# Kernel tuning notes

Measured on AMD Instinct MI355X. Metric: run time of the kernel, lower is better.

The kernel has to match this reference:

```python
import jax, jax.numpy as jnp
import numpy as np

B, T, D_MODEL = 2, 1024, 512
EXPAND = 2
D_INNER = D_MODEL * EXPAND
STATE = 16
K_CONV = 4


def setup_inputs() -> dict:
    key = jax.random.key(0)
    ks = jax.random.split(key, 10)
    sc = lambda k, shape: jax.random.normal(k, shape, jnp.float32) * 0.02
    return {
        "x": jax.random.normal(ks[0], (B, T, D_MODEL), jnp.float32),
        "ln_g": jnp.ones((D_MODEL,), jnp.float32),
        "ln_b": jnp.zeros((D_MODEL,), jnp.float32),
        "W_in": sc(ks[1], (2 * D_INNER, D_MODEL)),
        "conv_w": sc(ks[2], (D_INNER, 1, K_CONV)),
        "conv_b": jnp.zeros((D_INNER,), jnp.float32),
        "W_B": sc(ks[3], (STATE, D_INNER)),
        "W_C": sc(ks[4], (STATE, D_INNER)),
        "W_dt": sc(ks[5], (D_INNER, D_INNER)),
        "b_dt": jax.random.uniform(ks[6], (D_INNER,), jnp.float32, -4.0, -1.0),
        # log_A init: A_diag = -(n+1) from HiPPO, log(-A_diag) = log(n+1), broadcast over d_inner
        "log_A": jnp.broadcast_to(jnp.log(jnp.arange(1, STATE + 1, dtype=jnp.float32)), (D_INNER, STATE)),
        "W_out": sc(ks[7], (D_MODEL, D_INNER)),
    }


def _silu(v):
    return v * jax.nn.sigmoid(v)


def reference(x, ln_g, ln_b, W_in, conv_w, conv_b, W_B, W_C, W_dt, b_dt, log_A, W_out):
    residual = x
    # LayerNorm (biased variance, eps=1e-5)
    mu = x.mean(-1, keepdims=True)
    var = x.var(-1, keepdims=True)
    xn = (x - mu) * jax.lax.rsqrt(var + 1e-5) * ln_g + ln_b
    # input projection and gate split
    xz = xn @ W_in.T                      # (B,T,2*D_INNER)
    x_main, z = jnp.split(xz, 2, axis=-1)
    # depthwise causal conv1d (padding=3 then slice to T == left-pad 3)
    xc = jnp.transpose(x_main, (0, 2, 1))  # (B,D_INNER,T)
    xc = jax.lax.conv_general_dilated(
        xc, conv_w, window_strides=(1,), padding=[(K_CONV - 1, 0)],
        dimension_numbers=("NCH", "OIH", "NCH"), feature_group_count=D_INNER,
    ) + conv_b[None, :, None]
    x_main = _silu(jnp.transpose(xc, (0, 2, 1)))  # (B,T,D_INNER)
    # selective scan in fp32
    xf = x_main.astype(jnp.float32)
    Bt = xf @ W_B.T                        # (B,T,N)
    Ct = xf @ W_C.T                        # (B,T,N)
    dt = jax.nn.softplus(xf @ W_dt.T + b_dt)  # (B,T,D_INNER)
    A = -jnp.exp(log_A)                    # (D_INNER,N)
    dA = jnp.exp(A[None, None] * dt[..., None])              # (B,T,D_INNER,N)
    dBx = dt[..., None] * Bt[:, :, None, :] * xf[..., None]  # (B,T,D_INNER,N)

    def comb(c1, c2):
        a1, b1 = c1
        a2, b2 = c2
        return a1 * a2, a2 * b1 + b2

    _, h = jax.lax.associative_scan(comb, (dA, dBx), axis=1)  # h_t = dA_t*h_{t-1}+dBx_t
    y = (h * Ct[:, :, None, :]).sum(-1).astype(x.dtype)       # (B,T,D_INNER)
    out = (y * _silu(z)) @ W_out.T
    return residual + out
```

## Files before the change

kernel.cpp:

```cpp
#include <hip/hip_runtime.h>

#define T_SEQ 1024
#define DM 512
#define DI 1024
#define NS 16
#define NC 64
#define CL 16

typedef __attribute__((ext_vector_type(8))) short short8;
typedef __attribute__((ext_vector_type(4))) float f32x4;
typedef unsigned short u16;
typedef unsigned int u32;

__device__ inline float b2f(u16 u) {
    unsigned v = ((unsigned)u) << 16;
    return __builtin_bit_cast(float, v);
}
__device__ inline u16 f2b(float f) {
    unsigned u = __builtin_bit_cast(unsigned, f);
    u += 0x7fff + ((u >> 16) & 1);
    return (u16)(u >> 16);
}

__device__ inline void g2l16(const u16* g, short* l) {
    __builtin_amdgcn_global_load_lds((const __attribute__((address_space(1))) u32*)g,
                                     (__attribute__((address_space(3))) u32*)l, 16, 0, 0);
}

__global__ __launch_bounds__(256) void prep_k(const float* __restrict__ Win, const float* __restrict__ Wdt,
                       const float* __restrict__ Wout, const float* __restrict__ Wb,
                       const float* __restrict__ Wc,
                       u16* __restrict__ oWin, u16* __restrict__ oWdt, u16* __restrict__ oWout,
                       u16* __restrict__ oWb, u16* __restrict__ oWc,
                       const float* __restrict__ x, const float* __restrict__ g,
                       const float* __restrict__ be, u16* __restrict__ xn) {
    if (blockIdx.x < 2592) {
        int i = blockIdx.x * 256 + threadIdx.x;
        const float* s; u16* d; int off;
        if (i < 262144)      { s = Win;  d = oWin;  off = i; }
        else if (i < 524288) { s = Wdt;  d = oWdt;  off = i - 262144; }
        else if (i < 655360) { s = Wout; d = oWout; off = i - 524288; }
        else if (i < 659456) { s = Wb;   d = oWb;   off = i - 655360; }
        else                 { s = Wc;   d = oWc;   off = i - 659456; }
        float4 v = ((const float4*)s)[off];
        d[off * 4 + 0] = f2b(v.x);
        d[off * 4 + 1] = f2b(v.y);
        d[off * 4 + 2] = f2b(v.z);
        d[off * 4 + 3] = f2b(v.w);
        return;
    }
    int row = blockIdx.x - 2592, tid = threadIdx.x;
    float2 v = ((const float2*)(x + row * DM))[tid];
    float s = v.x + v.y, q = v.x * v.x + v.y * v.y;
    #pragma unroll
    for (int m = 1; m < 64; m <<= 1) { s += __shfl_xor(s, m); q += __shfl_xor(q, m); }
    __shared__ float ss[4], qq[4];
    if ((tid & 63) == 0) { ss[tid >> 6] = s; qq[tid >> 6] = q; }
    __syncthreads();
    s = ss[0] + ss[1] + ss[2] + ss[3];
    q = qq[0] + qq[1] + qq[2] + qq[3];
    float mu = s / DM;
    float var = q / DM - mu * mu;
    float rs = rsqrtf(var + 1e-5f);
    int c = tid * 2;
    xn[row * DM + c]     = f2b((v.x - mu) * rs * g[c] + be[c]);
    xn[row * DM + c + 1] = f2b((v.y - mu) * rs * g[c + 1] + be[c + 1]);
}

template<int BM, int BN, int NT, int EPI>
__global__ __launch_bounds__(256) void gemm_bt(const u16* __restrict__ A, int lda,
                                               const u16* __restrict__ Bw, int ldb,
                                               void* __restrict__ outp, int ldo,
                                               const float* __restrict__ extra) {
    __shared__ short a_sh[2][BM * 64];
    __shared__ short b_sh[2][BN * 64];
    constexpr int MI = BM / 32, NJ = BN / 32;
    int tid = threadIdx.x, w = tid >> 6, lane = tid & 63;
    int m0 = blockIdx.x * BM, n0 = blockIdx.y * BN;
    int wr = (w >> 1) * (BM / 2), wc = (w & 1) * (BN / 2);
    int lr = lane & 15, kg = lane >> 4;
    f32x4 acc[MI][NJ] = {};
    const u16* Abase = A + (size_t)m0 * lda;
    const u16* Bbase = Bw + (size_t)n0 * ldb;
    int lrow = lane >> 3;
    int lchunk = lane & 7;
    int schunk = lchunk ^ lrow;

    auto stage = [&](int cur, int kt) {
        int k0 = kt * 64;
        #pragma unroll
        for (int r = 0; r < BM / 32; ++r) {
            int row = r * 32 + w * 8 + lrow;
            g2l16(Abase + (size_t)row * lda + k0 + schunk * 8,
                  &a_sh[cur][(r * 32 + w * 8) * 64 + lane * 8]);
        }
        #pragma unroll
        for (int r = 0; r < BN / 32; ++r) {
            int row = r * 32 + w * 8 + lrow;
            g2l16(Bbase + (size_t)row * ldb + k0 + schunk * 8,
                  &b_sh[cur][(r * 32 + w * 8) * 64 + lane * 8]);
        }
    };

    stage(0, 0);
    __syncthreads();
    int cur = 0;
    for (int t = 0; t < NT; ++t) {
        if (t + 1 < NT) stage(cur ^ 1, t + 1);
        #pragma unroll
        for (int kk = 0; kk < 2; ++kk) {
            short8 af[MI], bfr[NJ];
            #pragma unroll
            for (int i = 0; i < MI; ++i) {
                int row = wr + i * 16 + lr;
                af[i] = *(const short8*)&a_sh[cur][row * 64 + (((kk << 2) | kg) ^ (row & 7)) * 8];
            }
            #pragma unroll
            for (int j = 0; j < NJ; ++j) {
                int row = wc + j * 16 + lr;
                bfr[j] = *(const short8*)&b_sh[cur][row * 64 + (((kk << 2) | kg) ^ (row & 7)) * 8];
            }
            #pragma unroll
            for (int i = 0; i < MI; ++i)
                #pragma unroll
                for (int j = 0; j < NJ; ++j)
                    acc[i][j] = __builtin_amdgcn_mfma_f32_16x16x32_bf16(af[i], bfr[j], acc[i][j], 0, 0, 0);
        }
        __syncthreads();
        cur ^= 1;
    }

    int rb = (lane >> 4) * 4, cc = lane & 15;
    #pragma unroll
    for (int i = 0; i < MI; ++i) {
        #pragma unroll
        for (int j = 0; j < NJ; ++j) {
            #pragma unroll
            for (int r = 0; r < 4; ++r) {
                int row = m0 + wr + i * 16 + rb + r;
                int col = n0 + wc + j * 16 + cc;
                float v = acc[i][j][r];
                if (EPI == 0) {
                    ((u16*)outp)[(size_t)row * ldo + col] = f2b(v);
                } else if (EPI == 1) {
                    float xx = v + extra[col];
                    float sp = (xx > 20.f) ? xx : log1pf(__expf(xx));
                    ((u16*)outp)[(size_t)row * ldo + col] = f2b(sp);
                } else {
                    ((float*)outp)[(size_t)row * ldo + col] = v + extra[(size_t)row * ldo + col];
                }
            }
        }
    }
}

__global__ void conv_k(const u16* __restrict__ xz, const float* __restrict__ w,
                       const float* __restrict__ cb, u16* __restrict__ xf) {
    int idx = blockIdx.x * 256 + threadIdx.x;
    int d = idx & (DI - 1);
    int bt = idx >> 10;
    int t = bt & (T_SEQ - 1);
    float s = cb[d];
    #pragma unroll
    for (int i = 0; i < 4; ++i) {
        int tt = t - 3 + i;
        if (tt >= 0) s += w[d * 4 + i] * b2f(xz[(size_t)(bt - 3 + i) * 2048 + d]);
    }
    float sig = 1.f / (1.f + __expf(-s));
    xf[idx] = f2b(s * sig);
}

__global__ __launch_bounds__(256) void bc_k(const u16* __restrict__ xf, const u16* __restrict__ Wb,
                                            const u16* __restrict__ Wc,
                                            float* __restrict__ Bt, float* __restrict__ Ct) {
    int m = blockIdx.x * 8 + (threadIdx.x >> 5);
    int j = threadIdx.x & 31;
    const u16* wrow = (j < 16) ? (Wb + j * DI) : (Wc + (j - 16) * DI);
    const short8* xr = (const short8*)(xf + (size_t)m * DI);
    const short8* wr = (const short8*)wrow;
    float s = 0.f;
    #pragma unroll 4
    for (int k = 0; k < DI / 8; ++k) {
        short8 a = xr[k], b = wr[k];
        #pragma unroll
        for (int e = 0; e < 8; ++e) s += b2f((u16)a[e]) * b2f((u16)b[e]);
    }
    float* o = (j < 16) ? Bt : Ct;
    o[(size_t)m * NS + (j & 15)] = s;
}

__global__ __launch_bounds__(256) void scanA(const u16* __restrict__ dt, const u16* __restrict__ xf,
                                             const float* __restrict__ Bt, const float* __restrict__ logA,
                                             float* __restrict__ Aprod, float* __restrict__ S) {
    int tid = threadIdx.x;
    int dblk = blockIdx.x & 3;
    int c = (blockIdx.x >> 2) & (NC - 1);
    int b = blockIdx.x >> 8;
    int d = dblk * 256 + tid;
    float Adn[NS], ap[NS], h[NS];
    #pragma unroll
    for (int j = 0; j < 4; ++j)
        *(float4*)&Adn[j * 4] = ((const float4*)(logA + (size_t)d * NS))[j];
    #pragma unroll
    for (int n = 0; n < NS; ++n) { Adn[n] = -__expf(Adn[n]); ap[n] = 1.f; h[n] = 0.f; }
    const u16* dtp = dt + ((size_t)b * T_SEQ + c * CL) * DI + d;
    const u16* xfp = xf + ((size_t)b * T_SEQ + c * CL) * DI + d;
    const float* Bp = Bt + ((size_t)b * T_SEQ + c * CL) * NS;
    #pragma unroll
    for (int i = 0; i < CL; ++i) {
        float dtv = b2f(dtp[(size_t)i * DI]);
        float xv  = b2f(xfp[(size_t)i * DI]);
        float ux = dtv * xv;
        float Bv[NS];
        #pragma unroll
        for (int j = 0; j < 4; ++j) *(float4*)&Bv[j * 4] = ((const float4*)(Bp + (size_t)i * NS))[j];
        #pragma unroll
        for (int n = 0; n < NS; ++n) {
            float dA = __expf(Adn[n] * dtv);
            h[n] = fmaf(dA, h[n], ux * Bv[n]);
            ap[n] *= dA;
        }
    }
    size_t o = ((((size_t)c * 2 + b) * DI) + d) * NS;
    #pragma unroll
    for (int j = 0; j < 4; ++j) {
        ((float4*)(Aprod + o))[j] = *(float4*)&ap[j * 4];
        ((float4*)(S + o))[j]     = *(float4*)&h[j * 4];
    }
}

__global__ __launch_bounds__(256) void scanB(const float* __restrict__ Aprod, const float* __restrict__ S,
                                             float* __restrict__ Hin) {
    int chain = blockIdx.x * 256 + threadIdx.x;
    float h = 0.f;
    #pragma unroll 8
    for (int c = 0; c < NC; ++c) {
        size_t o = (size_t)c * 32768 + chain;
        Hin[o] = h;
        h = fmaf(Aprod[o], h, S[o]);
    }
}

__global__ __launch_bounds__(256) void scanC(const u16* __restrict__ dt, const u16* __restrict__ xf,
                                             const float* __restrict__ Bt, const float* __restrict__ Ct,
                                             const float* __restrict__ logA, const float* __restrict__ Hin,
                                             const u16* __restrict__ xz, u16* __restrict__ ym) {
    int tid = threadIdx.x;
    int dblk = blockIdx.x & 3;
    int c = (blockIdx.x >> 2) & (NC - 1);
    int b = blockIdx.x >> 8;
    int d = dblk * 256 + tid;
    float Adn[NS], h[NS];
    #pragma unroll
    for (int j = 0; j < 4; ++j)
        *(float4*)&Adn[j * 4] = ((const float4*)(logA + (size_t)d * NS))[j];
    #pragma unroll
    for (int n = 0; n < NS; ++n) Adn[n] = -__expf(Adn[n]);
    size_t o = ((((size_t)c * 2 + b) * DI) + d) * NS;
    #pragma unroll
    for (int j = 0; j < 4; ++j) *(float4*)&h[j * 4] = ((const float4*)(Hin + o))[j];
    const u16* dtp = dt + ((size_t)b * T_SEQ + c * CL) * DI + d;
    const u16* xfp = xf + ((size_t)b * T_SEQ + c * CL) * DI + d;
    const float* Bp = Bt + ((size_t)b * T_SEQ + c * CL) * NS;
    const float* Cp = Ct + ((size_t)b * T_SEQ + c * CL) * NS;
    const u16* zp = xz + ((size_t)b * T_SEQ + c * CL) * 2048 + 1024 + d;
    u16* yp = ym + ((size_t)b * T_SEQ + c * CL) * DI + d;
    #pragma unroll
    for (int i = 0; i < CL; ++i) {
        float dtv = b2f(dtp[(size_t)i * DI]);
        float xv  = b2f(xfp[(size_t)i * DI]);
        float ux = dtv * xv;
        float Bv[NS], Cv[NS];
        #pragma unroll
        for (int j = 0; j < 4; ++j) {
            *(float4*)&Bv[j * 4] = ((const float4*)(Bp + (size_t)i * NS))[j];
            *(float4*)&Cv[j * 4] = ((const float4*)(Cp + (size_t)i * NS))[j];
        }
        float r = 0.f;
        #pragma unroll
        for (int n = 0; n < NS; ++n) {
            float dA = __expf(Adn[n] * dtv);
            h[n] = fmaf(dA, h[n], ux * Bv[n]);
            r = fmaf(h[n], Cv[n], r);
        }
        float zv = b2f(zp[(size_t)i * 2048]);
        float sz = zv / (1.f + __expf(-zv));
        yp[(size_t)i * DI] = f2b(r * sz);
    }
}

extern "C" void kernel_launch(void* const* d_in, const int* in_sizes, int n_in,
                              void* d_out, int out_size, void* d_ws, size_t ws_size,
                              hipStream_t stream) {
    const float* x     = (const float*)d_in[0];
    const float* ln_g  = (const float*)d_in[1];
    const float* ln_b  = (const float*)d_in[2];
    const float* W_in  = (const float*)d_in[3];
    const float* conv_w= (const float*)d_in[4];
    const float* conv_b= (const float*)d_in[5];
    const float* W_B   = (const float*)d_in[6];
    const float* W_C   = (const float*)d_in[7];
    const float* W_dt  = (const float*)d_in[8];
    const float* b_dt  = (const float*)d_in[9];
    const float* log_A = (const float*)d_in[10];
    const float* W_out = (const float*)d_in[11];

    char* ws = (char*)d_ws;
    u16* wInB  = (u16*)(ws + 0);
    u16* wDtB  = (u16*)(ws + 2097152);
    u16* wOutB = (u16*)(ws + 4194304);
    u16* wBB   = (u16*)(ws + 5242880);
    u16* wCB   = (u16*)(ws + 5275648);
    u16* xnB   = (u16*)(ws + 5308416);
    u16* xzB   = (u16*)(ws + 7405568);
    u16* xfB   = (u16*)(ws + 15794176);
    u16* dtB   = (u16*)(ws + 19988480);
    float* BtF = (float*)(ws + 24182784);
    float* CtF = (float*)(ws + 24313856);
    u16* ymB   = (u16*)(ws + 24444928);
    float* ApF = (float*)(ws + 28639232);
    float* SF  = (float*)(ws + 37027840);
    float* HiF = (float*)(ws + 45416448);

    prep_k<<<4640, 256, 0, stream>>>(W_in, W_dt, W_out, W_B, W_C, wInB, wDtB, wOutB, wBB, wCB,
                                     x, ln_g, ln_b, xnB);
    gemm_bt<64, 64, 8, 0><<<dim3(32, 32), 256, 0, stream>>>(xnB, 512, wInB, 512, (void*)xzB, 2048, nullptr);
    conv_k<<<8192, 256, 0, stream>>>(xzB, conv_w, conv_b, xfB);
    gemm_bt<64, 64, 16, 1><<<dim3(32, 16), 256, 0, stream>>>(xfB, 1024, wDtB, 1024, (void*)dtB, 1024, b_dt);
    bc_k<<<256, 256, 0, stream>>>(xfB, wBB, wCB, BtF, CtF);
    scanA<<<512, 256, 0, stream>>>(dtB, xfB, BtF, log_A, ApF, SF);
    scanB<<<128, 256, 0, stream>>>(ApF, SF, HiF);
    scanC<<<512, 256, 0, stream>>>(dtB, xfB, BtF, CtF, log_A, HiF, xzB, ymB);
    gemm_bt<32, 64, 16, 2><<<dim3(64, 8), 256, 0, stream>>>(ymB, 1024, wOutB, 1024, d_out, 512, x);
}
```

Measured before the change: 126.7 us.

## Use 128x128 GEMM tiles, fuse dt GEMM with B/C projection, lengthen scan chunks

GEMM tiles grow from 64x64 (or 32x64) to 128x128, and the barrier/waitcnt sequence is hand-written so the next stage's loads can overlap the current MFMAs. The dt GEMM and the B/C projection now run in one launch, with block index deciding which path each block takes. Scan chunks double in length and halve in count, so scanA and scanC launch fewer blocks and scanB has fewer carry steps. The trade-off is fewer workgroups on a large-CU GPU: the output GEMM drops to 64 blocks and the scans to 256, so occupancy and load balance may suffer.

Measured after the change: 141.8 us. +11.9%, slower.

```diff
diff --git a/kernel.cpp b/kernel.cpp
--- a/kernel.cpp
+++ b/kernel.cpp
@@ -4,8 +4,8 @@
 #define DM 512
 #define DI 1024
 #define NS 16
-#define NC 64
-#define CL 16
+#define NC 32
+#define CL 32
 
 typedef __attribute__((ext_vector_type(8))) short short8;
 typedef __attribute__((ext_vector_type(4))) float f32x4;
@@ -22,7 +22,7 @@
     return (u16)(u >> 16);
 }
 
-__device__ inline void g2l16(const u16* g, short* l) {
+__device__ inline void g2l16(const u16* g, const short* l) {
     __builtin_amdgcn_global_load_lds((const __attribute__((address_space(1))) u32*)g,
                                      (__attribute__((address_space(3))) u32*)l, 16, 0, 0);
 }
@@ -67,74 +67,76 @@
     xn[row * DM + c + 1] = f2b((v.y - mu) * rs * g[c + 1] + be[c + 1]);
 }
 
-template<int BM, int BN, int NT, int EPI>
-__global__ __launch_bounds__(256) void gemm_bt(const u16* __restrict__ A, int lda,
-                                               const u16* __restrict__ Bw, int ldb,
-                                               void* __restrict__ outp, int ldo,
-                                               const float* __restrict__ extra) {
-    __shared__ short a_sh[2][BM * 64];
-    __shared__ short b_sh[2][BN * 64];
-    constexpr int MI = BM / 32, NJ = BN / 32;
+template<int NT, int EPI>
+__device__ __forceinline__ void gemm_body(int bx, int by,
+        const u16* __restrict__ A, int lda, const u16* __restrict__ Bw, int ldb,
+        void* __restrict__ outp, int ldo, const float* __restrict__ extra,
+        short* a_sh, short* b_sh) {
     int tid = threadIdx.x, w = tid >> 6, lane = tid & 63;
-    int m0 = blockIdx.x * BM, n0 = blockIdx.y * BN;
-    int wr = (w >> 1) * (BM / 2), wc = (w & 1) * (BN / 2);
+    int m0 = bx * 128, n0 = by * 128;
+    int wr = (w >> 1) * 64, wc = (w & 1) * 64;
     int lr = lane & 15, kg = lane >> 4;
-    f32x4 acc[MI][NJ] = {};
+    f32x4 acc[4][4] = {};
     const u16* Abase = A + (size_t)m0 * lda;
     const u16* Bbase = Bw + (size_t)n0 * ldb;
-    int lrow = lane >> 3;
-    int lchunk = lane & 7;
-    int schunk = lchunk ^ lrow;
-
-    auto stage = [&](int cur, int kt) {
+    int r0 = tid >> 3, cl = tid & 7;
+
+    auto stage = [&](int buf, int kt) {
         int k0 = kt * 64;
         #pragma unroll
-        for (int r = 0; r < BM / 32; ++r) {
-            int row = r * 32 + w * 8 + lrow;
-            g2l16(Abase + (size_t)row * lda + k0 + schunk * 8,
-                  &a_sh[cur][(r * 32 + w * 8) * 64 + lane * 8]);
-        }
-        #pragma unroll
-        for (int r = 0; r < BN / 32; ++r) {
-            int row = r * 32 + w * 8 + lrow;
-            g2l16(Bbase + (size_t)row * ldb + k0 + schunk * 8,
-                  &b_sh[cur][(r * 32 + w * 8) * 64 + lane * 8]);
+        for (int r = 0; r < 4; ++r) {
+            int row = r * 32 + r0;
+            int sc = cl ^ (row & 7);
+            g2l16(Abase + (size_t)row * lda + k0 + sc * 8, a_sh + buf * 8192 + r * 2048 + w * 512);
+        }
+        #pragma unroll
+        for (int r = 0; r < 4; ++r) {
+            int row = r * 32 + r0;
+            int sc = cl ^ (row & 7);
+            g2l16(Bbase + (size_t)row * ldb + k0 + sc * 8, b_sh + buf * 8192 + r * 2048 + w * 512);
         }
     };
 
     stage(0, 0);
-    __syncthreads();
     int cur = 0;
     for (int t = 0; t < NT; ++t) {
-        if (t + 1 < NT) stage(cur ^ 1, t + 1);
+        if (t + 1 < NT) {
+            stage(cur ^ 1, t + 1);
+            asm volatile("s_waitcnt vmcnt(8)" ::: "memory");
+        } else {
+            asm volatile("s_waitcnt vmcnt(0)" ::: "memory");
+        }
+        asm volatile("s_barrier" ::: "memory");
+        const short* as = a_sh + cur * 8192;
+        const short* bs = b_sh + cur * 8192;
         #pragma unroll
         for (int kk = 0; kk < 2; ++kk) {
-            short8 af[MI], bfr[NJ];
+            short8 af[4], bfr[4];
             #pragma unroll
-            for (int i = 0; i < MI; ++i) {
+            for (int i = 0; i < 4; ++i) {
                 int row = wr + i * 16 + lr;
-                af[i] = *(const short8*)&a_sh[cur][row * 64 + (((kk << 2) | kg) ^ (row & 7)) * 8];
+                af[i] = *(const short8*)&as[row * 64 + ((kk * 4 + kg) ^ (lr & 7)) * 8];
             }
             #pragma unroll
-            for (int j = 0; j < NJ; ++j) {
+            for (int j = 0; j < 4; ++j) {
                 int row = wc + j * 16 + lr;
-                bfr[j] = *(const short8*)&b_sh[cur][row * 64 + (((kk << 2) | kg) ^ (row & 7)) * 8];
+                bfr[j] = *(const short8*)&bs[row * 64 + ((kk * 4 + kg) ^ (lr & 7)) * 8];
             }
             #pragma unroll
-            for (int i = 0; i < MI; ++i)
+            for (int i = 0; i < 4; ++i)
                 #pragma unroll
-                for (int j = 0; j < NJ; ++j)
+                for (int j = 0; j < 4; ++j)
                     acc[i][j] = __builtin_amdgcn_mfma_f32_16x16x32_bf16(af[i], bfr[j], acc[i][j], 0, 0, 0);
         }
-        __syncthreads();
+        asm volatile("s_barrier" ::: "memory");
         cur ^= 1;
     }
 
     int rb = (lane >> 4) * 4, cc = lane & 15;
     #pragma unroll
-    for (int i = 0; i < MI; ++i) {
-        #pragma unroll
-        for (int j = 0; j < NJ; ++j) {
+    for (int i = 0; i < 4; ++i) {
+        #pragma unroll
+        for (int j = 0; j < 4; ++j) {
             #pragma unroll
             for (int r = 0; r < 4; ++r) {
                 int row = m0 + wr + i * 16 + rb + r;
@@ -154,6 +156,43 @@
     }
 }
 
+template<int NT, int EPI>
+__global__ __launch_bounds__(256) void gemm_bt(const u16* __restrict__ A, int lda,
+                                               const u16* __restrict__ Bw, int ldb,
+                                               void* __restrict__ outp, int ldo,
+                                               const float* __restrict__ extra) {
+    __shared__ short a_sh[2 * 128 * 64];
+    __shared__ short b_sh[2 * 128 * 64];
+    gemm_body<NT, EPI>(blockIdx.x, blockIdx.y, A, lda, Bw, ldb, outp, ldo, extra, a_sh, b_sh);
+}
+
+__global__ __launch_bounds__(256) void gemm1_bc(const u16* __restrict__ xf, const u16* __restrict__ Wdt,
+                                                const float* __restrict__ b_dt, u16* __restrict__ dt,
+                                                const u16* __restrict__ Wb, const u16* __restrict__ Wc,
+                                                float* __restrict__ Bt, float* __restrict__ Ct) {
+    __shared__ short a_sh[2 * 128 * 64];
+    __shared__ short b_sh[2 * 128 * 64];
+    int bid = blockIdx.x;
+    if (bid < 128) {
+        gemm_body<16, 1>(bid & 15, bid >> 4, xf, DI, Wdt, DI, (void*)dt, DI, b_dt, a_sh, b_sh);
+        return;
+    }
+    int m = (bid - 128) * 8 + (threadIdx.x >> 5);
+    int j = threadIdx.x & 31;
+    const u16* wrow = (j < 16) ? (Wb + j * DI) : (Wc + (j - 16) * DI);
+    const short8* xr = (const short8*)(xf + (size_t)m * DI);
+    const short8* wrp = (const short8*)wrow;
+    float s = 0.f;
+    #pragma unroll 4
+    for (int k = 0; k < DI / 8; ++k) {
+        short8 a = xr[k], b = wrp[k];
+        #pragma unroll
+        for (int e = 0; e < 8; ++e) s += b2f((u16)a[e]) * b2f((u16)b[e]);
+    }
+    float* o = (j < 16) ? Bt : Ct;
+    o[(size_t)m * NS + (j & 15)] = s;
+}
+
 __global__ void conv_k(const u16* __restrict__ xz, const float* __restrict__ w,
                        const float* __restrict__ cb, u16* __restrict__ xf) {
     int idx = blockIdx.x * 256 + threadIdx.x;
@@ -170,32 +209,13 @@
     xf[idx] = f2b(s * sig);
 }
 
-__global__ __launch_bounds__(256) void bc_k(const u16* __restrict__ xf, const u16* __restrict__ Wb,
-                                            const u16* __restrict__ Wc,
-                                            float* __restrict__ Bt, float* __restrict__ Ct) {
-    int m = blockIdx.x * 8 + (threadIdx.x >> 5);
-    int j = threadIdx.x & 31;
-    const u16* wrow = (j < 16) ? (Wb + j * DI) : (Wc + (j - 16) * DI);
-    const short8* xr = (const short8*)(xf + (size_t)m * DI);
-    const short8* wr = (const short8*)wrow;
-    float s = 0.f;
-    #pragma unroll 4
-    for (int k = 0; k < DI / 8; ++k) {
-        short8 a = xr[k], b = wr[k];
-        #pragma unroll
-        for (int e = 0; e < 8; ++e) s += b2f((u16)a[e]) * b2f((u16)b[e]);
-    }
-    float* o = (j < 16) ? Bt : Ct;
-    o[(size_t)m * NS + (j & 15)] = s;
-}
-
 __global__ __launch_bounds__(256) void scanA(const u16* __restrict__ dt, const u16* __restrict__ xf,
                                              const float* __restrict__ Bt, const float* __restrict__ logA,
                                              float* __restrict__ Aprod, float* __restrict__ S) {
     int tid = threadIdx.x;
     int dblk = blockIdx.x & 3;
     int c = (blockIdx.x >> 2) & (NC - 1);
-    int b = blockIdx.x >> 8;
+    int b = blockIdx.x >> 7;
     int d = dblk * 256 + tid;
     float Adn[NS], ap[NS], h[NS];
     #pragma unroll
@@ -206,7 +226,7 @@
     const u16* dtp = dt + ((size_t)b * T_SEQ + c * CL) * DI + d;
     const u16* xfp = xf + ((size_t)b * T_SEQ + c * CL) * DI + d;
     const float* Bp = Bt + ((size_t)b * T_SEQ + c * CL) * NS;
-    #pragma unroll
+    #pragma unroll 8
     for (int i = 0; i < CL; ++i) {
         float dtv = b2f(dtp[(size_t)i * DI]);
         float xv  = b2f(xfp[(size_t)i * DI]);
@@ -248,7 +268,7 @@
     int tid = threadIdx.x;
     int dblk = blockIdx.x & 3;
     int c = (blockIdx.x >> 2) & (NC - 1);
-    int b = blockIdx.x >> 8;
+    int b = blockIdx.x >> 7;
     int d = dblk * 256 + tid;
     float Adn[NS], h[NS];
     #pragma unroll
@@ -265,7 +285,7 @@
     const float* Cp = Ct + ((size_t)b * T_SEQ + c * CL) * NS;
     const u16* zp = xz + ((size_t)b * T_SEQ + c * CL) * 2048 + 1024 + d;
     u16* yp = ym + ((size_t)b * T_SEQ + c * CL) * DI + d;
-    #pragma unroll
+    #pragma unroll 8
     for (int i = 0; i < CL; ++i) {
         float dtv = b2f(dtp[(size_t)i * DI]);
         float xv  = b2f(xfp[(size_t)i * DI]);
@@ -324,12 +344,11 @@
 
     prep_k<<<4640, 256, 0, stream>>>(W_in, W_dt, W_out, W_B, W_C, wInB, wDtB, wOutB, wBB, wCB,
                                      x, ln_g, ln_b, xnB);
-    gemm_bt<64, 64, 8, 0><<<dim3(32, 32), 256, 0, stream>>>(xnB, 512, wInB, 512, (void*)xzB, 2048, nullptr);
+    gemm_bt<8, 0><<<dim3(16, 16), 256, 0, stream>>>(xnB, 512, wInB, 512, (void*)xzB, 2048, nullptr);
     conv_k<<<8192, 256, 0, stream>>>(xzB, conv_w, conv_b, xfB);
-    gemm_bt<64, 64, 16, 1><<<dim3(32, 16), 256, 0, stream>>>(xfB, 1024, wDtB, 1024, (void*)dtB, 1024, b_dt);
-    bc_k<<<256, 256, 0, stream>>>(xfB, wBB, wCB, BtF, CtF);
-    scanA<<<512, 256, 0, stream>>>(dtB, xfB, BtF, log_A, ApF, SF);
+    gemm1_bc<<<384, 256, 0, stream>>>(xfB, wDtB, b_dt, dtB, wBB, wCB, BtF, CtF);
+    scanA<<<256, 256, 0, stream>>>(dtB, xfB, BtF, log_A, ApF, SF);
     scanB<<<128, 256, 0, stream>>>(ApF, SF, HiF);
-    scanC<<<512, 256, 0, stream>>>(dtB, xfB, BtF, CtF, log_A, HiF, xzB, ymB);
-    gemm_bt<32, 64, 16, 2><<<dim3(64, 8), 256, 0, stream>>>(ymB, 1024, wOutB, 1024, d_out, 512, x);
-}
+    scanC<<<256, 256, 0, stream>>>(dtB, xfB, BtF, CtF, log_A, HiF, xzB, ymB);
+    gemm_bt<16, 2><<<dim3(16, 4), 256, 0, stream>>>(ymB, 1024, wOutB, 1024, d_out, 512, x);
+}
```
